# Performance work log

Measured on AMD Instinct MI355X. Metric: run time of the kernel, lower is better.

The kernel has to match this reference:

```python
import jax, jax.numpy as jnp
import numpy as np
from jax import lax

WINDOW_SIZE = 11
SIGMA = 1.5
C1 = 0.01 ** 2
C2 = 0.03 ** 2


def _gaussian_window(window_size, sigma, channel):
    # 1D gaussian, normalized, then outer product -> 2D window
    x = np.arange(window_size) - window_size // 2
    g = np.exp(-(x.astype(np.float64) ** 2) / (2.0 * sigma ** 2))
    g = (g / g.sum()).astype(np.float32)
    w2d = np.outer(g, g)  # [K, K]
    # depthwise kernel [C, 1, K, K] (OIHW with feature_group_count=C)
    w = np.broadcast_to(w2d, (channel, 1, window_size, window_size))
    return jnp.asarray(np.ascontiguousarray(w))


def _depthwise_conv(x, w, channel):
    pad = WINDOW_SIZE // 2
    return lax.conv_general_dilated(
        x, w,
        window_strides=(1, 1),
        padding=[(pad, pad), (pad, pad)],
        dimension_numbers=("NCHW", "OIHW", "NCHW"),
        feature_group_count=channel,
    )


def setup_inputs() -> dict:
    key = jax.random.key(0)
    k1, k2 = jax.random.split(key)
    B, C, H, W = 32, 3, 512, 512
    img1 = jax.random.uniform(k1, (B, C, H, W), dtype=jnp.float32)
    img2 = jax.random.uniform(k2, (B, C, H, W), dtype=jnp.float32)
    return {"img1": img1, "img2": img2}


def reference(img1, img2):
    channel = img1.shape[1]
    window = _gaussian_window(WINDOW_SIZE, SIGMA, channel)

    mu1 = _depthwise_conv(img1, window, channel)
    mu2 = _depthwise_conv(img2, window, channel)

    mu1_sq = mu1 * mu1
    mu2_sq = mu2 * mu2
    mu1_mu2 = mu1 * mu2

    sigma1_sq = _depthwise_conv(img1 * img1, window, channel) - mu1_sq
    sigma2_sq = _depthwise_conv(img2 * img2, window, channel) - mu2_sq
    sigma12 = _depthwise_conv(img1 * img2, window, channel) - mu1_mu2

    sigma1_sq = jnp.maximum(sigma1_sq, 0.0)
    sigma2_sq = jnp.maximum(sigma2_sq, 0.0)

    numerator = (2.0 * mu1_mu2 + C1) * (2.0 * sigma12 + C2)
    denominator = (mu1_sq + mu2_sq + C1) * (sigma1_sq + sigma2_sq + C2)
    ssim_map = jnp.clip(numerator / denominator, 0.0, 1.0)

    return 1.0 - jnp.mean(ssim_map)
```

## Files before the change

kernel.cpp:

```cpp
#include <hip/hip_runtime.h>


typedef float v2f __attribute__((ext_vector_type(2)));
typedef float v4f __attribute__((ext_vector_type(4)));

constexpr int IMG    = 512;
constexpr int TPB    = 256;
constexpr int SH     = 64;
constexpr int NPAIR  = 37;
constexpr int LW     = 272;
constexpr int PLANES = 32 * 3;
constexpr double N_PIX = 25165824.0;

__global__ __launch_bounds__(TPB, 3) void ssim_map_kernel(
    const float* __restrict__ img1, const float* __restrict__ img2,
    double* __restrict__ partial)
{
    constexpr float GW[11] = {
        0.0010283801f, 0.0075987583f, 0.0360007721f, 0.1093607008f,
        0.2130055439f, 0.2660117257f, 0.2130055439f, 0.1093607008f,
        0.0360007721f, 0.0075987583f, 0.0010283801f };
    constexpr float GWp[13] = {
        0.0f,
        0.0010283801f, 0.0075987583f, 0.0360007721f, 0.1093607008f,
        0.2130055439f, 0.2660117257f, 0.2130055439f, 0.1093607008f,
        0.0360007721f, 0.0075987583f, 0.0010283801f,
        0.0f };

    __shared__ v4f  sbuf[3][LW];
    __shared__ float wsum[TPB / 64];

    const int tid   = threadIdx.x;
    const int x0    = blockIdx.x * TPB;
    const int y0    = blockIdx.y * SH;
    const int plane = blockIdx.z;

    const float* p1 = img1 + (size_t)plane * IMG * IMG;
    const float* p2 = img2 + (size_t)plane * IMG * IMG;

    const int  c   = x0 + tid - 8;
    const bool cok = (unsigned)c < (unsigned)IMG;
    const int  c2  = x0 + 248 + tid;
    const bool c2ok = (unsigned)c2 < (unsigned)IMG;

    v2f rg1[6], rg2[6], rg11[6], rg22[6], rg12[6];

    v2f accv = {0.0f, 0.0f};

    float pa1, pb1, pa2, pb2, qa1, qb1, qa2, qb2;
    auto prefetch = [&](int i) {
        const int  rA  = y0 - 5 + 2 * i;
        const int  rB  = rA + 1;
        const bool aok = (unsigned)rA < (unsigned)IMG;
        const bool bok = (unsigned)rB < (unsigned)IMG;
        const size_t oA = (size_t)rA * IMG;
        const size_t oB = (size_t)rB * IMG;
        pa1 = (aok && cok) ? p1[oA + c] : 0.0f;
        pb1 = (bok && cok) ? p1[oB + c] : 0.0f;
        pa2 = (aok && cok) ? p2[oA + c] : 0.0f;
        pb2 = (bok && cok) ? p2[oB + c] : 0.0f;
        if (tid < 16) {
            qa1 = (aok && c2ok) ? p1[oA + c2] : 0.0f;
            qb1 = (bok && c2ok) ? p1[oB + c2] : 0.0f;
            qa2 = (aok && c2ok) ? p2[oA + c2] : 0.0f;
            qb2 = (bok && c2ok) ? p2[oB + c2] : 0.0f;
        }
    };

    prefetch(0);

    for (int ib = 0; ib < NPAIR; ib += 6) {
#pragma unroll
        for (int j = 0; j < 6; ++j) {
            const int i = ib + j;
            if (i < NPAIR) {
                sbuf[j % 3][tid] = v4f{pa1, pb1, pa2, pb2};
                if (tid < 16) sbuf[j % 3][256 + tid] = v4f{qa1, qb1, qa2, qb2};

                if (i + 1 < NPAIR) prefetch(i + 1);

                __syncthreads();

                v2f a1 = {0,0}, a2 = {0,0}, a11 = {0,0}, a22 = {0,0}, a12 = {0,0};
                const v4f* sp = &sbuf[j % 3][tid + 3];
#pragma unroll
                for (int k = 0; k < 11; ++k) {
                    const v4f s  = sp[k];
                    const v2f x1 = __builtin_shufflevector(s, s, 0, 1);
                    const v2f x2 = __builtin_shufflevector(s, s, 2, 3);
                    const float g = GW[k];
                    const v2f t1 = g * x1;
                    const v2f t2 = g * x2;
                    a1 += t1;
                    a2 += t2;
                    a11 = __builtin_elementwise_fma(t1, x1, a11);
                    a22 = __builtin_elementwise_fma(t2, x2, a22);
                    a12 = __builtin_elementwise_fma(t1, x2, a12);
                }
                rg1[j] = a1;  rg2[j] = a2;
                rg11[j] = a11; rg22[j] = a22; rg12[j] = a12;
            }

            if (i >= 5 && i < NPAIR) {
                v2f sx1={0,0}, sy1={0,0}, sx2={0,0}, sy2={0,0};
                v2f sx11={0,0}, sy11={0,0}, sx22={0,0}, sy22={0,0};
                v2f sx12={0,0}, sy12={0,0};
#pragma unroll
                for (int m = 0; m < 6; ++m) {
                    const int s = (j + 1 + m) % 6;
                    const v2f wx = { GWp[2*m + 1], GWp[2*m + 2] };
                    const v2f wy = { GWp[2*m],     GWp[2*m + 1] };
                    sx1  = __builtin_elementwise_fma(wx, rg1[s],  sx1);
                    sy1  = __builtin_elementwise_fma(wy, rg1[s],  sy1);
                    sx2  = __builtin_elementwise_fma(wx, rg2[s],  sx2);
                    sy2  = __builtin_elementwise_fma(wy, rg2[s],  sy2);
                    sx11 = __builtin_elementwise_fma(wx, rg11[s], sx11);
                    sy11 = __builtin_elementwise_fma(wy, rg11[s], sy11);
                    sx22 = __builtin_elementwise_fma(wx, rg22[s], sx22);
                    sy22 = __builtin_elementwise_fma(wy, rg22[s], sy22);
                    sx12 = __builtin_elementwise_fma(wx, rg12[s], sx12);
                    sy12 = __builtin_elementwise_fma(wy, rg12[s], sy12);
                }
                const v2f m1  = { sx1.x + sx1.y,  sy1.x + sy1.y };
                const v2f m2  = { sx2.x + sx2.y,  sy2.x + sy2.y };
                const v2f e11 = { sx11.x + sx11.y, sy11.x + sy11.y };
                const v2f e22 = { sx22.x + sx22.y, sy22.x + sy22.y };
                const v2f e12 = { sx12.x + sx12.y, sy12.x + sy12.y };

                const v2f mu11 = m1 * m1;
                const v2f mu22 = m2 * m2;
                const v2f mu12 = m1 * m2;
                const v2f zero = {0.0f, 0.0f};
                const v2f one  = {1.0f, 1.0f};
                const v2f sg1  = __builtin_elementwise_max(e11 - mu11, zero);
                const v2f sg2  = __builtin_elementwise_max(e22 - mu22, zero);
                const v2f sg12 = e12 - mu12;
                const v2f num = (2.0f * mu12 + 1e-4f) * (2.0f * sg12 + 9e-4f);
                const v2f den = (mu11 + mu22 + 1e-4f) * (sg1 + sg2 + 9e-4f);
                v2f v = { num.x * __builtin_amdgcn_rcpf(den.x),
                          num.y * __builtin_amdgcn_rcpf(den.y) };
                v = __builtin_elementwise_min(__builtin_elementwise_max(v, zero), one);
                accv += v;
            }
        }
    }

    float acc = accv.x + accv.y;
#pragma unroll
    for (int off = 32; off > 0; off >>= 1)
        acc += __shfl_down(acc, off, 64);
    if ((tid & 63) == 0) wsum[tid >> 6] = acc;
    __syncthreads();
    if (tid == 0) {
        double blocksum = 0.0;
#pragma unroll
        for (int w = 0; w < TPB / 64; ++w) blocksum += (double)wsum[w];
        atomicAdd(partial, blocksum);
    }
}

__global__ void ssim_finalize_kernel(const double* __restrict__ partial,
                                     float* __restrict__ out)
{
    out[0] = 1.0f - (float)(partial[0] / N_PIX);
}

extern "C" void kernel_launch(void* const* d_in, const int* in_sizes, int n_in,
                              void* d_out, int out_size, void* d_ws, size_t ws_size,
                              hipStream_t stream) {
    const float* img1 = (const float*)d_in[0];
    const float* img2 = (const float*)d_in[1];
    float* out = (float*)d_out;
    double* acc = (double*)d_ws;

    hipMemsetAsync(acc, 0, sizeof(double), stream);

    dim3 grid(IMG / TPB, IMG / SH, PLANES);
    ssim_map_kernel<<<grid, TPB, 0, stream>>>(img1, img2, acc);
    ssim_finalize_kernel<<<1, 1, 0, stream>>>(acc, out);
}
```

Before: 248.2 us.

## Raise occupancy, specialize interior row loads, replace atomics with per-block partials

Raises the launch-bounds occupancy hint from 3 to 6 blocks per SIMD/CU, which forces tighter register allocation. Adds a fast prefetch path for blocks away from the top and bottom image edges that skips the row bounds checks, and clamps column indices so loads are always in range. Replaces the global double atomicAdd and the memset with per-block partial sums written to workspace, then reduced by a 256-thread finalize kernel. The tighter register limit risks spills in the heavily unrolled convolution loops.

```diff
diff --git a/kernel.cpp b/kernel.cpp
--- a/kernel.cpp
+++ b/kernel.cpp
@@ -10,9 +10,10 @@
 constexpr int NPAIR  = 37;
 constexpr int LW     = 272;
 constexpr int PLANES = 32 * 3;
+constexpr int NBLK   = (IMG / TPB) * (IMG / SH) * PLANES;
 constexpr double N_PIX = 25165824.0;
 
-__global__ __launch_bounds__(TPB, 3) void ssim_map_kernel(
+__global__ __launch_bounds__(TPB, 6) void ssim_map_kernel(
     const float* __restrict__ img1, const float* __restrict__ img2,
     double* __restrict__ partial)
 {
@@ -34,40 +35,57 @@
     const int x0    = blockIdx.x * TPB;
     const int y0    = blockIdx.y * SH;
     const int plane = blockIdx.z;
+    const bool yedge = (blockIdx.y == 0) || (blockIdx.y == (IMG / SH - 1));
 
     const float* p1 = img1 + (size_t)plane * IMG * IMG;
     const float* p2 = img2 + (size_t)plane * IMG * IMG;
 
-    const int  c   = x0 + tid - 8;
-    const bool cok = (unsigned)c < (unsigned)IMG;
-    const int  c2  = x0 + 248 + tid;
+    const int  c    = x0 + tid - 8;
+    const bool cok  = (unsigned)c < (unsigned)IMG;
+    const int  cc   = cok ? c : 0;
+    const int  c2   = x0 + 248 + tid;
     const bool c2ok = (unsigned)c2 < (unsigned)IMG;
+    const int  cc2  = c2ok ? c2 : 0;
 
     v2f rg1[6], rg2[6], rg11[6], rg22[6], rg12[6];
-
     v2f accv = {0.0f, 0.0f};
 
     float pa1, pb1, pa2, pb2, qa1, qb1, qa2, qb2;
-    auto prefetch = [&](int i) {
+
+    auto prefetch_g = [&](int i) {
         const int  rA  = y0 - 5 + 2 * i;
         const int  rB  = rA + 1;
         const bool aok = (unsigned)rA < (unsigned)IMG;
         const bool bok = (unsigned)rB < (unsigned)IMG;
         const size_t oA = (size_t)rA * IMG;
         const size_t oB = (size_t)rB * IMG;
-        pa1 = (aok && cok) ? p1[oA + c] : 0.0f;
-        pb1 = (bok && cok) ? p1[oB + c] : 0.0f;
-        pa2 = (aok && cok) ? p2[oA + c] : 0.0f;
-        pb2 = (bok && cok) ? p2[oB + c] : 0.0f;
+        pa1 = (aok && cok) ? p1[oA + cc] : 0.0f;
+        pb1 = (bok && cok) ? p1[oB + cc] : 0.0f;
+        pa2 = (aok && cok) ? p2[oA + cc] : 0.0f;
+        pb2 = (bok && cok) ? p2[oB + cc] : 0.0f;
         if (tid < 16) {
-            qa1 = (aok && c2ok) ? p1[oA + c2] : 0.0f;
-            qb1 = (bok && c2ok) ? p1[oB + c2] : 0.0f;
-            qa2 = (aok && c2ok) ? p2[oA + c2] : 0.0f;
-            qb2 = (bok && c2ok) ? p2[oB + c2] : 0.0f;
+            qa1 = (aok && c2ok) ? p1[oA + cc2] : 0.0f;
+            qb1 = (bok && c2ok) ? p1[oB + cc2] : 0.0f;
+            qa2 = (aok && c2ok) ? p2[oA + cc2] : 0.0f;
+            qb2 = (bok && c2ok) ? p2[oB + cc2] : 0.0f;
         }
     };
-
-    prefetch(0);
+    auto prefetch_f = [&](int i) {
+        const size_t oA = (size_t)(y0 - 5 + 2 * i) * IMG;
+        const size_t oB = oA + IMG;
+        pa1 = cok ? p1[oA + cc] : 0.0f;
+        pb1 = cok ? p1[oB + cc] : 0.0f;
+        pa2 = cok ? p2[oA + cc] : 0.0f;
+        pb2 = cok ? p2[oB + cc] : 0.0f;
+        if (tid < 16) {
+            qa1 = c2ok ? p1[oA + cc2] : 0.0f;
+            qb1 = c2ok ? p1[oB + cc2] : 0.0f;
+            qa2 = c2ok ? p2[oA + cc2] : 0.0f;
+            qb2 = c2ok ? p2[oB + cc2] : 0.0f;
+        }
+    };
+
+    if (yedge) prefetch_g(0); else prefetch_f(0);
 
     for (int ib = 0; ib < NPAIR; ib += 6) {
 #pragma unroll
@@ -77,7 +95,9 @@
                 sbuf[j % 3][tid] = v4f{pa1, pb1, pa2, pb2};
                 if (tid < 16) sbuf[j % 3][256 + tid] = v4f{qa1, qb1, qa2, qb2};
 
-                if (i + 1 < NPAIR) prefetch(i + 1);
+                if (i + 1 < NPAIR) {
+                    if (yedge) prefetch_g(i + 1); else prefetch_f(i + 1);
+                }
 
                 __syncthreads();
 
@@ -155,14 +175,28 @@
         double blocksum = 0.0;
 #pragma unroll
         for (int w = 0; w < TPB / 64; ++w) blocksum += (double)wsum[w];
-        atomicAdd(partial, blocksum);
+        const int bid = blockIdx.x + (IMG / TPB) * (blockIdx.y + (IMG / SH) * blockIdx.z);
+        partial[bid] = blocksum;
     }
 }
 
-__global__ void ssim_finalize_kernel(const double* __restrict__ partial,
-                                     float* __restrict__ out)
+__global__ __launch_bounds__(256) void ssim_finalize_kernel(
+    const double* __restrict__ partial, float* __restrict__ out)
 {
-    out[0] = 1.0f - (float)(partial[0] / N_PIX);
+    __shared__ double wsum[4];
+    const int tid = threadIdx.x;
+    double s = 0.0;
+#pragma unroll
+    for (int k = 0; k < NBLK / 256; ++k) s += partial[tid + 256 * k];
+#pragma unroll
+    for (int off = 32; off > 0; off >>= 1)
+        s += __shfl_down(s, off, 64);
+    if ((tid & 63) == 0) wsum[tid >> 6] = s;
+    __syncthreads();
+    if (tid == 0) {
+        double t = wsum[0] + wsum[1] + wsum[2] + wsum[3];
+        out[0] = 1.0f - (float)(t / N_PIX);
+    }
 }
 
 extern "C" void kernel_launch(void* const* d_in, const int* in_sizes, int n_in,
@@ -171,11 +205,9 @@
     const float* img1 = (const float*)d_in[0];
     const float* img2 = (const float*)d_in[1];
     float* out = (float*)d_out;
-    double* acc = (double*)d_ws;
-
-    hipMemsetAsync(acc, 0, sizeof(double), stream);
+    double* parts = (double*)d_ws;
 
     dim3 grid(IMG / TPB, IMG / SH, PLANES);
-    ssim_map_kernel<<<grid, TPB, 0, stream>>>(img1, img2, acc);
-    ssim_finalize_kernel<<<1, 1, 0, stream>>>(acc, out);
+    ssim_map_kernel<<<grid, TPB, 0, stream>>>(img1, img2, parts);
+    ssim_finalize_kernel<<<1, 256, 0, stream>>>(parts, out);
 }
```

Measured after the change: 416.1 us. 1.68x slower.
